# Optimization experiments

Measured on AMD Instinct MI355X. Metric: run time of the kernel, lower is better.

Reference implementation:

```python
import jax, jax.numpy as jnp
import numpy as np

B, N, F, E, C, FC = 16, 5000, 512, 160000, 64, 128


def gcn_conv(x, src, dst, W, b, n_total):
    loop = jnp.arange(n_total, dtype=src.dtype)
    s = jnp.concatenate([src, loop])
    d = jnp.concatenate([dst, loop])
    deg = jax.ops.segment_sum(jnp.ones_like(s, dtype=x.dtype), d, num_segments=n_total)
    dinv = jnp.where(deg > 0, jax.lax.rsqrt(deg), 0.0)
    norm = dinv[s] * dinv[d]                      # [E']
    h = x @ W                                      # [n_total, out]
    msg = h[s] * norm[:, None]
    out = jax.ops.segment_sum(msg, d, num_segments=n_total)
    return out + b


def setup_inputs() -> dict:
    key = jax.random.key(0)
    ks = jax.random.split(key, 12)
    inp = {
        "node_features": jax.random.normal(ks[0], (B, N, F), jnp.float32),
        "col_features": jax.random.normal(ks[1], (B, C, FC), jnp.float32),
        "edge_index": jax.random.randint(ks[2], (2, E), 0, N, dtype=jnp.int64),
        # GCNConv 1/2 weights + node head
        "W1": jax.random.normal(ks[3], (F, 16), jnp.float32) / np.sqrt(F),
        "b1": jnp.zeros((16,), jnp.float32),
        "W2": jax.random.normal(ks[4], (16, 16), jnp.float32) / 4.0,
        "b2": jnp.zeros((16,), jnp.float32),
        "fc_w": jax.random.normal(ks[5], (16, 1), jnp.float32) / 4.0,
        "fc_b": jnp.zeros((1,), jnp.float32),
        # column MLP: Linear(FC,16) -> ReLU -> Linear(16,1)
        "cw1": jax.random.normal(ks[6], (FC, 16), jnp.float32) / np.sqrt(FC),
        "cb1": jnp.zeros((16,), jnp.float32),
        "cw2": jax.random.normal(ks[7], (16, 1), jnp.float32) / 4.0,
        "cb2": jnp.zeros((1,), jnp.float32),
    }
    return inp


def reference(node_features, col_features, edge_index, W1, b1, W2, b2, fc_w, fc_b, cw1, cb1, cw2, cb2):
    b, n, _ = node_features.shape
    n_total = b * n
    # batched edge_index via node-offset trick (shared graph per batch element)
    offsets = (jnp.arange(b, dtype=edge_index.dtype) * n)[:, None]   # [B,1]
    src = (edge_index[0][None, :] + offsets).reshape(-1)              # [B*E]
    dst = (edge_index[1][None, :] + offsets).reshape(-1)

    x = node_features.reshape(n_total, -1)
    x = jax.nn.relu(gcn_conv(x, src, dst, W1, b1, n_total))
    x = jax.nn.relu(gcn_conv(x, src, dst, W2, b2, n_total))
    node_logits = (x.reshape(b, n, 16) @ fc_w + fc_b)[..., 0]         # [B,N]

    h = jax.nn.relu(col_features @ cw1 + cb1)
    col_logits = (h @ cw2 + cb2)[..., 0]                              # [B,C]

    joint = node_logits[:, :, None] + col_logits[:, None, :]          # [B,N,C]
    return joint.reshape(b, -1)                                       # [B, N*C]
```

## Files before the change

### kernel.cpp

```cpp
#include <hip/hip_runtime.h>
#include <hip/hip_bf16.h>

typedef unsigned short u16;
typedef unsigned int   u32;
typedef __attribute__((ext_vector_type(8))) short bf16x8;
typedef __attribute__((ext_vector_type(4))) float f32x4;

#define B_  16
#define N_  5000
#define F_  512
#define C_  64
#define FC_ 128
#define NT  (B_ * N_)

__device__ __forceinline__ float bf2f(u16 h) {
    return __uint_as_float(((u32)h) << 16);
}
__device__ __forceinline__ u16 f2bf(float f) {
    union { __hip_bfloat16 h; u16 s; } c; c.h = __float2bfloat16(f); return c.s;
}
__device__ __forceinline__ float ldw(const void* p, int i, int fF) {
    return fF ? bf2f(((const u16*)p)[i]) : ((const float*)p)[i];
}

__global__ __launch_bounds__(256) void det_k(const u32* __restrict__ x32,
                                             const u32* __restrict__ ei32,
                                             int* __restrict__ flags)
{
    __shared__ int cnt;
    __shared__ int orv;
    if (threadIdx.x == 0) { cnt = 0; orv = 0; }
    __syncthreads();
    u32 w = x32[threadIdx.x];
    int e = (int)((w >> 7) & 0xffu);
    if (e >= 112 && e <= 136) atomicAdd(&cnt, 1);
    if (threadIdx.x < 32) {
        if (ei32[2 * threadIdx.x + 1] != 0u) atomicOr(&orv, 1);
    }
    __syncthreads();
    if (threadIdx.x == 0) {
        flags[0] = (cnt >= 128) ? 1 : 0;
        flags[1] = (orv == 0) ? 1 : 0;
    }
}

__device__ __forceinline__ int src_at(const u32* ei32, int t, int E, int fI) {
    return (int)(fI ? ei32[2 * t] : ei32[t]);
}
__device__ __forceinline__ int dst_at(const u32* ei32, int t, int E, int fI) {
    return (int)(fI ? ei32[2 * (E + t)] : ei32[E + t]);
}

__global__ __launch_bounds__(256) void prep_weights(
    const void* __restrict__ W1, const void* __restrict__ W2,
    const void* __restrict__ fcw, const void* __restrict__ cw1,
    const void* __restrict__ cw2, const void* __restrict__ b1,
    const void* __restrict__ b2, const void* __restrict__ fcb,
    const void* __restrict__ cb1, const void* __restrict__ cb2,
    const int* __restrict__ flags,
    float* __restrict__ w1f, float* __restrict__ w2f, float* __restrict__ fcwf,
    float* __restrict__ cw1f, float* __restrict__ cw2f, float* __restrict__ b1f,
    float* __restrict__ b2f, float* __restrict__ fcbf, float* __restrict__ cb1f,
    float* __restrict__ cb2f, u16* __restrict__ w1b)
{
    int fF = flags[0];
    int t = blockIdx.x * blockDim.x + threadIdx.x;
    if (t < 8192) { w1f[t] = ldw(W1, t, fF); return; }
    int u = t - 8192;
    if (u < 256)  { w2f[u]  = ldw(W2, u, fF);  return; }  u -= 256;
    if (u < 16)   { fcwf[u] = ldw(fcw, u, fF); return; }  u -= 16;
    if (u < 2048) { cw1f[u] = ldw(cw1, u, fF); return; }  u -= 2048;
    if (u < 16)   { cw2f[u] = ldw(cw2, u, fF); return; }  u -= 16;
    if (u < 16)   { b1f[u]  = ldw(b1, u, fF);  return; }  u -= 16;
    if (u < 16)   { b2f[u]  = ldw(b2, u, fF);  return; }  u -= 16;
    if (u < 1)    { fcbf[u] = ldw(fcb, u, fF); return; }  u -= 1;
    if (u < 16)   { cb1f[u] = ldw(cb1, u, fF); return; }  u -= 16;
    if (u < 1)    { cb2f[u] = ldw(cb2, u, fF); return; }  u -= 1;
    if (u < 8192) {
        int kb = u >> 9;
        int r  = (u >> 3) & 63;
        int j  = u & 7;
        w1b[u] = f2bf(ldw(W1, (kb * 32 + (r >> 4) * 8 + j) * 16 + (r & 15), fF));
    }
}

__global__ __launch_bounds__(256) void deg_k(const u32* __restrict__ ei32,
                                             const int* __restrict__ flags,
                                             int* __restrict__ deg, int E)
{
    int t = blockIdx.x * blockDim.x + threadIdx.x;
    if (t >= E) return;
    int d = dst_at(ei32, t, E, flags[1]);
    if ((unsigned)d < (unsigned)N_) atomicAdd(&deg[d], 1);
}

__global__ __launch_bounds__(1024) void scan_k(const int* __restrict__ deg,
                                               int* __restrict__ rowptr,
                                               int* __restrict__ cursor,
                                               float* __restrict__ dinv)
{
    __shared__ int ssum[1024];
    int t = threadIdx.x;
    int base = t * 5;
    int loc[5];
    int run = 0;
#pragma unroll
    for (int i = 0; i < 5; i++) {
        int idx = base + i;
        int v = (idx < N_) ? deg[idx] : 0;
        loc[i] = run;
        run += v;
    }
    ssum[t] = run;
    __syncthreads();
    for (int offs = 1; offs < 1024; offs <<= 1) {
        int v = (t >= offs) ? ssum[t - offs] : 0;
        __syncthreads();
        ssum[t] += v;
        __syncthreads();
    }
    int exclusive = ssum[t] - run;
#pragma unroll
    for (int i = 0; i < 5; i++) {
        int idx = base + i;
        if (idx < N_) {
            int rp = exclusive + loc[i];
            rowptr[idx] = rp;
            cursor[idx] = rp;
            dinv[idx] = 1.0f / sqrtf((float)deg[idx] + 1.0f);
        }
    }
    if (t == 1023) rowptr[N_] = ssum[1023];
}

__global__ __launch_bounds__(256) void fill_k(const u32* __restrict__ ei32,
                                              const int* __restrict__ flags,
                                              int* __restrict__ cursor,
                                              int* __restrict__ csr, int E)
{
    int t = blockIdx.x * blockDim.x + threadIdx.x;
    if (t >= E) return;
    int fI = flags[1];
    int s = src_at(ei32, t, E, fI);
    int d = dst_at(ei32, t, E, fI);
    if ((unsigned)d >= (unsigned)N_) return;
    if ((unsigned)s >= (unsigned)N_) s = 0;
    int pos = atomicAdd(&cursor[d], 1);
    if ((unsigned)pos < (unsigned)E) csr[pos] = s;
}

__global__ __launch_bounds__(256) void gemm1_k(const void* __restrict__ xraw,
                                               const float* __restrict__ w1f,
                                               const u16* __restrict__ w1b,
                                               const float* __restrict__ dinv,
                                               const int* __restrict__ flags,
                                               u16* __restrict__ out)
{
    __shared__ float smem[4352];
    const int t    = threadIdx.x;
    const int lane = t & 63;
    const int wv   = t >> 6;
    const int row0 = blockIdx.x * 64;
    const int fF   = flags[0];

    if (fF) {
        const u16* xb = (const u16*)xraw;
        bf16x8 bfr[16];
#pragma unroll
        for (int kb = 0; kb < 16; kb++)
            bfr[kb] = *(const bf16x8*)(w1b + kb * 512 + lane * 8);

        f32x4 acc = {0.0f, 0.0f, 0.0f, 0.0f};
        const u16* xr = xb + (size_t)(row0 + wv * 16 + (lane & 15)) * F_
                           + (lane >> 4) * 8;
#pragma unroll
        for (int kb = 0; kb < 16; kb++) {
            bf16x8 a = *(const bf16x8*)(xr + kb * 32);
            acc = __builtin_amdgcn_mfma_f32_16x16x32_bf16(a, bfr[kb], acc, 0, 0, 0);
        }
#pragma unroll
        for (int i = 0; i < 4; i++) {
            int grow = row0 + wv * 16 + (lane >> 4) * 4 + i;
            int n  = grow % N_;
            int bb = grow / N_;
            out[(size_t)n * 256 + bb * 16 + (lane & 15)] = f2bf(acc[i] * dinv[n]);
        }
        return;
    }

    float acc[16];
#pragma unroll
    for (int k = 0; k < 16; k++) acc[k] = 0.0f;

    for (int c = 0; c < 8; c++) {
        __syncthreads();
        const float* xf = (const float*)xraw + c * 64;
#pragma unroll
        for (int i = 0; i < 4; i++) {
            int u = i * 256 + t;
            int r = u >> 4, c4 = u & 15;
            float4 v = *(const float4*)(xf + (size_t)(row0 + r) * F_ + c4 * 4);
            float* dp = &smem[r * 65 + c4 * 4];
            dp[0] = v.x; dp[1] = v.y; dp[2] = v.z; dp[3] = v.w;
        }
        __syncthreads();
        const float* xr = &smem[lane * 65 + wv * 16];
        const float* wr = w1f + (c * 64 + wv * 16) * 16;
#pragma unroll
        for (int f = 0; f < 16; f++) {
            float xv = xr[f];
#pragma unroll
            for (int k = 0; k < 16; k++) acc[k] += xv * wr[f * 16 + k];
        }
    }

    __syncthreads();
    float (*red)[64][17] = (float (*)[64][17])smem;
#pragma unroll
    for (int k = 0; k < 16; k++) red[wv][lane][k] = acc[k];
    __syncthreads();

    int r  = t >> 2;
    int kc = (t & 3) * 4;
    int row = row0 + r;
    int n = row % N_;
    int b = row / N_;
    float s = dinv[n];
    union { uint2 u; u16 h[4]; } o;
#pragma unroll
    for (int k = 0; k < 4; k++) {
        float v = red[0][r][kc + k] + red[1][r][kc + k]
                + red[2][r][kc + k] + red[3][r][kc + k];
        o.h[k] = f2bf(v * s);
    }
    *(uint2*)(out + (size_t)n * 256 + b * 16 + kc) = o.u;
}

__global__ __launch_bounds__(256) void agg1_k(const u16* __restrict__ h,
                                              const int* __restrict__ rowptr,
                                              const int* __restrict__ csr,
                                              const float* __restrict__ dinv,
                                              const float* __restrict__ b1f,
                                              const float* __restrict__ w2f,
                                              u16* __restrict__ out)
{
    int d   = blockIdx.x;
    int tid = threadIdx.x;
    int k   = tid & 15;
    float acc = bf2f(h[(size_t)d * 256 + tid]);
    int e0 = rowptr[d], e1 = rowptr[d + 1];
    for (int base = e0; base < e1; base += 8) {
        int idx[8];
#pragma unroll
        for (int j = 0; j < 8; j++) {
            int e = base + j;
            idx[j] = csr[e < e1 ? e : e0];
        }
        float v[8];
#pragma unroll
        for (int j = 0; j < 8; j++) v[j] = bf2f(h[(size_t)idx[j] * 256 + tid]);
#pragma unroll
        for (int j = 0; j < 8; j++) if (base + j < e1) acc += v[j];
    }
    float dv = dinv[d];
    float x1 = fmaxf(acc * dv + b1f[k], 0.0f);
    float h2 = 0.0f;
#pragma unroll
    for (int j = 0; j < 16; j++) {
        float xj = __shfl(x1, j, 16);
        h2 += xj * w2f[j * 16 + k];
    }
    out[(size_t)d * 256 + tid] = f2bf(h2 * dv);
}

__global__ __launch_bounds__(256) void agg2_k(const u16* __restrict__ h,
                                              const int* __restrict__ rowptr,
                                              const int* __restrict__ csr,
                                              const float* __restrict__ dinv,
                                              const float* __restrict__ b2f,
                                              const float* __restrict__ fcwf,
                                              const float* __restrict__ fcbf,
                                              float* __restrict__ nl)
{
    int d   = blockIdx.x;
    int tid = threadIdx.x;
    int k   = tid & 15;
    int b   = tid >> 4;
    float acc = bf2f(h[(size_t)d * 256 + tid]);
    int e0 = rowptr[d], e1 = rowptr[d + 1];
    for (int base = e0; base < e1; base += 8) {
        int idx[8];
#pragma unroll
        for (int j = 0; j < 8; j++) {
            int e = base + j;
            idx[j] = csr[e < e1 ? e : e0];
        }
        float v[8];
#pragma unroll
        for (int j = 0; j < 8; j++) v[j] = bf2f(h[(size_t)idx[j] * 256 + tid]);
#pragma unroll
        for (int j = 0; j < 8; j++) if (base + j < e1) acc += v[j];
    }
    float x2 = fmaxf(acc * dinv[d] + b2f[k], 0.0f);
    float p = x2 * fcwf[k];
    p += __shfl_xor(p, 8, 16);
    p += __shfl_xor(p, 4, 16);
    p += __shfl_xor(p, 2, 16);
    p += __shfl_xor(p, 1, 16);
    if (k == 0) nl[b * N_ + d] = p + fcbf[0];
}

__global__ __launch_bounds__(256) void col_k(const void* __restrict__ cfraw,
                                             const float* __restrict__ cw1f,
                                             const float* __restrict__ cb1f,
                                             const float* __restrict__ cw2f,
                                             const float* __restrict__ cb2f,
                                             const int* __restrict__ flags,
                                             float* __restrict__ cl)
{
    int t = blockIdx.x * blockDim.x + threadIdx.x;
    if (t >= B_ * C_) return;
    float acc[16];
#pragma unroll
    for (int k = 0; k < 16; k++) acc[k] = cb1f[k];
    if (flags[0]) {
        const u16* r = (const u16*)cfraw + (size_t)t * FC_;
        for (int f = 0; f < FC_; f += 8) {
            uint4 pk = *(const uint4*)(r + f);
            u32 q[4] = {pk.x, pk.y, pk.z, pk.w};
#pragma unroll
            for (int j = 0; j < 4; j++) {
                float v0 = bf2f((u16)(q[j] & 0xffffu));
                float v1 = bf2f((u16)(q[j] >> 16));
                const float* w0 = cw1f + (f + 2 * j) * 16;
#pragma unroll
                for (int k = 0; k < 16; k++) acc[k] += v0 * w0[k];
#pragma unroll
                for (int k = 0; k < 16; k++) acc[k] += v1 * w0[16 + k];
            }
        }
    } else {
        const float* r = (const float*)cfraw + (size_t)t * FC_;
        for (int f = 0; f < FC_; f += 4) {
            float4 a = *(const float4*)(r + f);
            float v[4] = {a.x, a.y, a.z, a.w};
#pragma unroll
            for (int j = 0; j < 4; j++) {
                const float* w0 = cw1f + (f + j) * 16;
#pragma unroll
                for (int k = 0; k < 16; k++) acc[k] += v[j] * w0[k];
            }
        }
    }
    float s = cb2f[0];
#pragma unroll
    for (int k = 0; k < 16; k++) s += fmaxf(acc[k], 0.0f) * cw2f[k];
    cl[t] = s;
}

__global__ __launch_bounds__(256) void join_k(const float* __restrict__ nl,
                                              const float* __restrict__ cl,
                                              const int* __restrict__ flags,
                                              void* __restrict__ outraw)
{
    int t = blockIdx.x * blockDim.x + threadIdx.x;
    if (t >= NT * C_ / 8) return;
    int g  = t >> 3;
    int c0 = (t & 7) * 8;
    int b  = g / N_;
    float nv = nl[g];
    const float* c = cl + b * C_ + c0;
    float4 a0 = *(const float4*)c;
    float4 a1 = *(const float4*)(c + 4);
    float v[8] = {a0.x, a0.y, a0.z, a0.w, a1.x, a1.y, a1.z, a1.w};
#pragma unroll
    for (int i = 0; i < 8; i++) v[i] += nv;
    size_t idx = (size_t)g * C_ + c0;
    if (flags[0]) {
        union { uint4 u; u16 h[8]; } pkv;
#pragma unroll
        for (int i = 0; i < 8; i++) pkv.h[i] = f2bf(v[i]);
        *(uint4*)((u16*)outraw + idx) = pkv.u;
    } else {
        float* o = (float*)outraw + idx;
        *(float4*)o       = make_float4(v[0], v[1], v[2], v[3]);
        *(float4*)(o + 4) = make_float4(v[4], v[5], v[6], v[7]);
    }
}

extern "C" void kernel_launch(void* const* d_in, const int* in_sizes, int n_in,
                              void* d_out, int out_size, void* d_ws, size_t ws_size,
                              hipStream_t stream)
{
    const void* x    = d_in[0];
    const void* cf   = d_in[1];
    const u32*  ei32 = (const u32*)d_in[2];
    const void* W1   = d_in[3];
    const void* b1   = d_in[4];
    const void* W2   = d_in[5];
    const void* b2   = d_in[6];
    const void* fcw  = d_in[7];
    const void* fcb  = d_in[8];
    const void* cw1  = d_in[9];
    const void* cb1  = d_in[10];
    const void* cw2  = d_in[11];
    const void* cb2  = d_in[12];

    const int E = in_sizes[2] / 2;

    char* base = (char*)d_ws;
    size_t off = 0;
    auto alloc = [&](size_t bytes) -> void* {
        void* p = base + off;
        off = (off + bytes + 255) & ~(size_t)255;
        return p;
    };
    int*   flags  = (int*)alloc(2 * 4);
    float* w1f  = (float*)alloc(8192 * 4);
    u16*   w1b  = (u16*)alloc(8192 * 2);
    float* w2f  = (float*)alloc(256 * 4);
    float* fcwf = (float*)alloc(16 * 4);
    float* cw1f = (float*)alloc(2048 * 4);
    float* cw2f = (float*)alloc(16 * 4);
    float* b1f  = (float*)alloc(16 * 4);
    float* b2f  = (float*)alloc(16 * 4);
    float* fcbf = (float*)alloc(4);
    float* cb1f = (float*)alloc(16 * 4);
    float* cb2f = (float*)alloc(4);
    int*   deg    = (int*)alloc((size_t)N_ * 4);
    int*   rowptr = (int*)alloc((size_t)(N_ + 1) * 4);
    int*   cursor = (int*)alloc((size_t)N_ * 4);
    float* dinv   = (float*)alloc((size_t)N_ * 4);
    int*   csr    = (int*)alloc((size_t)E * 4);
    u16*   bufA = (u16*)alloc((size_t)NT * 16 * 2);
    u16*   bufB = (u16*)alloc((size_t)NT * 16 * 2);
    float* nl   = (float*)alloc((size_t)NT * 4);
    float* cl   = (float*)alloc((size_t)B_ * C_ * 4);

    det_k<<<1, 256, 0, stream>>>((const u32*)x, ei32, flags);
    hipMemsetAsync(deg, 0, (size_t)N_ * 4, stream);
    prep_weights<<<(10578 + 8192 + 255) / 256, 256, 0, stream>>>(
        W1, W2, fcw, cw1, cw2, b1, b2, fcb, cb1, cb2, flags,
        w1f, w2f, fcwf, cw1f, cw2f, b1f, b2f, fcbf, cb1f, cb2f, w1b);
    deg_k<<<(E + 255) / 256, 256, 0, stream>>>(ei32, flags, deg, E);
    scan_k<<<1, 1024, 0, stream>>>(deg, rowptr, cursor, dinv);
    fill_k<<<(E + 255) / 256, 256, 0, stream>>>(ei32, flags, cursor, csr, E);

    gemm1_k<<<NT / 64, 256, 0, stream>>>(x, w1f, w1b, dinv, flags, bufA);
    agg1_k<<<N_, 256, 0, stream>>>(bufA, rowptr, csr, dinv, b1f, w2f, bufB);
    agg2_k<<<N_, 256, 0, stream>>>(bufB, rowptr, csr, dinv, b2f, fcwf, fcbf, nl);
    col_k<<<(B_ * C_ + 255) / 256, 256, 0, stream>>>(cf, cw1f, cb1f, cw2f, cb2f, flags, cl);
    join_k<<<(NT * C_ / 8 + 255) / 256, 256, 0, stream>>>(nl, cl, flags, d_out);
}
```

Baseline: 402.6 us.

## Double-buffer per-wave fp32 x tiles in gemm1 and drop block barriers

The fp32 path of gemm1 now gives each wave its own K-slice and its own double-buffered shared-memory tile. The next chunk is prefetched into registers while the current one is computed, so the per-chunk __syncthreads are removed. Shared-memory use grows to about 36KB per block, and the launch bounds ask for 4 blocks per CU. This only affects the fp32-input path; the bf16 MFMA path is unchanged.

```diff
diff --git a/kernel.cpp b/kernel.cpp
--- a/kernel.cpp
+++ b/kernel.cpp
@@ -149,14 +149,14 @@
     if ((unsigned)pos < (unsigned)E) csr[pos] = s;
 }
 
-__global__ __launch_bounds__(256) void gemm1_k(const void* __restrict__ xraw,
-                                               const float* __restrict__ w1f,
-                                               const u16* __restrict__ w1b,
-                                               const float* __restrict__ dinv,
-                                               const int* __restrict__ flags,
-                                               u16* __restrict__ out)
-{
-    __shared__ float smem[4352];
+__global__ __launch_bounds__(256, 4) void gemm1_k(const void* __restrict__ xraw,
+                                                  const float* __restrict__ w1f,
+                                                  const u16* __restrict__ w1b,
+                                                  const float* __restrict__ dinv,
+                                                  const int* __restrict__ flags,
+                                                  u16* __restrict__ out)
+{
+    __shared__ float smem[9216];
     const int t    = threadIdx.x;
     const int lane = t & 63;
     const int wv   = t >> 6;
@@ -192,26 +192,46 @@
 #pragma unroll
     for (int k = 0; k < 16; k++) acc[k] = 0.0f;
 
+    const int wvu  = __builtin_amdgcn_readfirstlane(wv);
+    float* wt      = smem + wvu * 2304;
+    const float* xf = (const float*)xraw;
+    const int rsub = lane >> 2;
+    const int slot = lane & 3;
+
+    float4 pre[4];
+    auto g1_load = [&](int cc) {
+#pragma unroll
+        for (int i = 0; i < 4; i++) {
+            int row = 16 * i + rsub;
+            pre[i] = *(const float4*)(xf + (size_t)(row0 + row) * F_
+                                      + wvu * 128 + cc * 16 + slot * 4);
+        }
+    };
+    auto g1_store = [&](int bb) {
+#pragma unroll
+        for (int i = 0; i < 4; i++) {
+            int row = 16 * i + rsub;
+            float* dp = wt + bb * 1152 + row * 18 + slot * 4;
+            *(float2*)dp       = make_float2(pre[i].x, pre[i].y);
+            *(float2*)(dp + 2) = make_float2(pre[i].z, pre[i].w);
+        }
+    };
+
+    g1_load(0);
+    g1_store(0);
     for (int c = 0; c < 8; c++) {
-        __syncthreads();
-        const float* xf = (const float*)xraw + c * 64;
-#pragma unroll
-        for (int i = 0; i < 4; i++) {
-            int u = i * 256 + t;
-            int r = u >> 4, c4 = u & 15;
-            float4 v = *(const float4*)(xf + (size_t)(row0 + r) * F_ + c4 * 4);
-            float* dp = &smem[r * 65 + c4 * 4];
-            dp[0] = v.x; dp[1] = v.y; dp[2] = v.z; dp[3] = v.w;
-        }
-        __syncthreads();
-        const float* xr = &smem[lane * 65 + wv * 16];
-        const float* wr = w1f + (c * 64 + wv * 16) * 16;
-#pragma unroll
-        for (int f = 0; f < 16; f++) {
-            float xv = xr[f];
-#pragma unroll
-            for (int k = 0; k < 16; k++) acc[k] += xv * wr[f * 16 + k];
-        }
+        if (c < 7) g1_load(c + 1);
+        const float* xrow = wt + (c & 1) * 1152 + lane * 18;
+        const float* wr   = w1f + (wvu * 128 + c * 16) * 16;
+#pragma unroll
+        for (int f = 0; f < 16; f += 2) {
+            float2 xv = *(const float2*)(xrow + f);
+#pragma unroll
+            for (int k = 0; k < 16; k++) acc[k] += xv.x * wr[f * 16 + k];
+#pragma unroll
+            for (int k = 0; k < 16; k++) acc[k] += xv.y * wr[(f + 1) * 16 + k];
+        }
+        if (c < 7) g1_store((c + 1) & 1);
     }
 
     __syncthreads();
```

Measured after the change: 362.8 us. 1.11x faster.
